# Kernel tuning notes

Hardware: AMD Instinct MI355X
Metric: run time of the kernel (lower is better)

Reference implementation:

```python
import jax, jax.numpy as jnp
import numpy as np

D_MODEL = 1024
EXPAND = 2
D_INNER = EXPAND * D_MODEL      # 2048
D_STATE = 2
D_CONV = 4
DT_RANK = (D_MODEL + 15) // 16  # 64
BATCH, SEQ = 2, 4096
LN_EPS = 1e-5


def setup_inputs() -> dict:
    key = jax.random.key(0)
    ks = jax.random.split(key, 16)
    s = 0.02
    inp = {
        "x":       jax.random.normal(ks[0], (BATCH, SEQ, D_MODEL), jnp.float32),
        # Mamba params (torch Linear convention: W is [out, in])
        "w_in":    jax.random.normal(ks[1], (2 * D_INNER, D_MODEL), jnp.float32) * s,
        "conv_w":  jax.random.normal(ks[2], (D_INNER, 1, D_CONV), jnp.float32) * s,
        "conv_b":  jnp.zeros((D_INNER,), jnp.float32),
        "w_xproj": jax.random.normal(ks[3], (DT_RANK + 2 * D_STATE, D_INNER), jnp.float32) * s,
        "w_dt":    jax.random.normal(ks[4], (D_INNER, DT_RANK), jnp.float32) * s,
        "b_dt":    jax.random.normal(ks[5], (D_INNER,), jnp.float32) * s - 4.0,  # softplus -> small dt
        "a_log":   jnp.log(jnp.broadcast_to(jnp.arange(1, D_STATE + 1, dtype=jnp.float32), (D_INNER, D_STATE))),
        "d_skip":  jnp.ones((D_INNER,), jnp.float32),
        "w_out":   jax.random.normal(ks[6], (D_MODEL, D_INNER), jnp.float32) * s,
        # LayerNorms
        "ln1_g":   jnp.ones((D_MODEL,), jnp.float32),
        "ln1_b":   jnp.zeros((D_MODEL,), jnp.float32),
        "ln2_g":   jnp.ones((D_MODEL,), jnp.float32),
        "ln2_b":   jnp.zeros((D_MODEL,), jnp.float32),
        # FFN (Linear d->d, ReLU, Linear d->d; dropout inactive at eval)
        "ffn_w1":  jax.random.normal(ks[7], (D_MODEL, D_MODEL), jnp.float32) * s,
        "ffn_b1":  jnp.zeros((D_MODEL,), jnp.float32),
        "ffn_w2":  jax.random.normal(ks[8], (D_MODEL, D_MODEL), jnp.float32) * s,
        "ffn_b2":  jnp.zeros((D_MODEL,), jnp.float32),
    }
    return inp


def _ln(x, g, b):
    mu = x.mean(-1, keepdims=True)
    v = ((x - mu) ** 2).mean(-1, keepdims=True)
    return (x - mu) * jax.lax.rsqrt(v + LN_EPS) * g + b


def _mamba(x, w_in, conv_w, conv_b, w_xproj, w_dt, b_dt, a_log, d_skip, w_out):
    Bsz = x.shape[0]
    xz = x @ w_in.T                      # (B,L,2*D_INNER)
    xp, z = jnp.split(xz, 2, axis=-1)
    # depthwise causal conv over time
    xc = jnp.transpose(xp, (0, 2, 1))    # (B,D,L)
    xc = jax.lax.conv_general_dilated(
        xc, conv_w, window_strides=(1,), padding=[(D_CONV - 1, 0)],
        feature_group_count=D_INNER)
    xc = xc + conv_b[None, :, None]
    xp = jax.nn.silu(jnp.transpose(xc, (0, 2, 1)))   # (B,L,D)
    # input-dependent SSM params
    x_dbl = xp @ w_xproj.T               # (B,L,DT_RANK+2N)
    dt, Bm, Cm = jnp.split(x_dbl, [DT_RANK, DT_RANK + D_STATE], axis=-1)
    dt = jax.nn.softplus(dt @ w_dt.T + b_dt)          # (B,L,D)
    A = -jnp.exp(a_log)                  # (D,N)
    dA = jnp.exp(dt[..., None] * A)                  # (B,L,D,N)
    dBu = dt[..., None] * Bm[:, :, None, :] * xp[..., None]  # (B,L,D,N)

    def step(h, inp):
        da, dbu, c = inp                 # (B,D,N),(B,D,N),(B,N)
        h = da * h + dbu
        y = jnp.einsum('bdn,bn->bd', h, c)
        return h, y

    h0 = jnp.zeros((Bsz, D_INNER, D_STATE), x.dtype)
    _, ys = jax.lax.scan(step, h0, (jnp.swapaxes(dA, 0, 1),
                                    jnp.swapaxes(dBu, 0, 1),
                                    jnp.swapaxes(Cm, 0, 1)))
    y = jnp.swapaxes(ys, 0, 1)           # (B,L,D)
    y = (y + d_skip * xp) * jax.nn.silu(z)
    return y @ w_out.T                   # (B,L,d_model)


def reference(x, w_in, conv_w, conv_b, w_xproj, w_dt, b_dt, a_log, d_skip, w_out,
              ln1_g, ln1_b, ln2_g, ln2_b, ffn_w1, ffn_b1, ffn_w2, ffn_b2):
    h = x + _mamba(_ln(x, ln1_g, ln1_b), w_in, conv_w, conv_b, w_xproj,
                   w_dt, b_dt, a_log, d_skip, w_out)
    f = _ln(h, ln2_g, ln2_b)
    f = jax.nn.relu(f @ ffn_w1.T + ffn_b1) @ ffn_w2.T + ffn_b2
    return h + f
```

## Files before the change

kernel.cpp:

```cpp
#include <hip/hip_runtime.h>

typedef unsigned short u16;
typedef __bf16 bf16x8 __attribute__((ext_vector_type(8)));
typedef float f32x4 __attribute__((ext_vector_type(4)));
typedef float f32x2 __attribute__((ext_vector_type(2)));
typedef u16 u16x4 __attribute__((ext_vector_type(4)));
typedef u16 u16x8 __attribute__((ext_vector_type(8)));

#define SEQ   4096
#define DM    1024
#define DI    2048
#define NTOK  8192
#define NXP   68
#define DTR   64
#define NCH   4096
#define CHUNK 32
#define NCHK  128

__device__ __forceinline__ float bf2f(u16 v) {
  union { unsigned u; float f; } x; x.u = ((unsigned)v) << 16; return x.f;
}
__device__ __forceinline__ u16 f2bf(float f) {
  unsigned u = __float_as_uint(f);
  return (u16)((u + 0x7FFFu + ((u >> 16) & 1u)) >> 16);
// ... 198 lines not shown
      bfr[j] = *reinterpret_cast<const bf16x8*>(
          &sB[cur][(wn + j * 16 + r) * 32 + (q ^ rsw) * 8]);
    if (kt + 1 < nk) {
      gA0 += 32; gA1 += 32; gB0 += 32; gB1 += 32;
      g2l16(gA0, lA0[cur ^ 1]); g2l16(gA1, lA1[cur ^ 1]);
      g2l16(gB0, lB0[cur ^ 1]); g2l16(gB1, lB1[cur ^ 1]);
    }
#pragma unroll
    for (int i = 0; i < 4; ++i)
#pragma unroll
      for (int j = 0; j < 4; ++j)
        acc[i][j] = __builtin_amdgcn_mfma_f32_16x16x32_bf16(af[i], bfr[j], acc[i][j], 0, 0, 0);
  }

  __syncthreads();
  float* ep = (wv < 2) ? ((float*)&sA[0][0] + wv * 2048)
                       : ((float*)&sB[0][0] + (wv - 2) * 2048);
  const int r2 = lane >> 2;
  const int ccol = ((lane & 3) ^ (r2 & 3)) * 16;

#pragma unroll
  for (int i = 0; i < 4; ++i) {
#pragma unroll
    for (int j = 0; j < 4; ++j)
#pragma unroll
      for (int t = 0; t < 4; ++t)
        ep[(q * 4 + t) * 68 + j * 16 + r] = acc[i][j][t];
    f32x4 w0 = *(const f32x4*)&ep[r2 * 68 + ccol + 0];
    f32x4 w1 = *(const f32x4*)&ep[r2 * 68 + ccol + 4];
    f32x4 w2 = *(const f32x4*)&ep[r2 * 68 + ccol + 8];
    f32x4 w3 = *(const f32x4*)&ep[r2 * 68 + ccol + 12];
    float vv[16];
#pragma unroll
    for (int k = 0; k < 4; ++k) {
      vv[k] = w0[k]; vv[4 + k] = w1[k]; vv[8 + k] = w2[k]; vv[12 + k] = w3[k];
    }
    const int row = m0 + wm + i * 16 + r2;
    const int colg = n0 + wn + ccol;
    const size_t idx = (size_t)row * N + colg;
    if (EPI == 2) {
      u16x8 b0 = *(const u16x8*)&bias[colg];
      u16x8 b1 = *(const u16x8*)&bias[colg + 8];
      u16x8 o0, o1;
#pragma unroll
      for (int k = 0; k < 8; ++k) {
        float v0 = vv[k] + bf2f(b0[k]);
        float v1 = vv[8 + k] + bf2f(b1[k]);
        v0 = (v0 > 15.f) ? v0 : __logf(1.f + __expf(v0));
        v1 = (v1 > 15.f) ? v1 : __logf(1.f + __expf(v1));
        o0[k] = f2bf(v0); o1[k] = f2bf(v1);
      }
      *(u16x8*)&((u16*)Cp)[idx] = o0;
      *(u16x8*)&((u16*)Cp)[idx + 8] = o1;
    } else if (EPI == 3) {
      float ax[16];
      if (fl) {
        f32x4 a0 = *(const f32x4*)&addf[idx];
        f32x4 a1 = *(const f32x4*)&addf[idx + 4];
        f32x4 a2 = *(const f32x4*)&addf[idx + 8];
        f32x4 a3 = *(const f32x4*)&addf[idx + 12];
#pragma unroll
        for (int k = 0; k < 4; ++k) {
          ax[k] = a0[k]; ax[4 + k] = a1[k]; ax[8 + k] = a2[k]; ax[12 + k] = a3[k];
        }
      } else {
        u16x8 a0 = *(const u16x8*)&addbf[idx];
        u16x8 a1 = *(const u16x8*)&addbf[idx + 8];
#pragma unroll
        for (int k = 0; k < 8; ++k) { ax[k] = bf2f(a0[k]); ax[8 + k] = bf2f(a1[k]); }
      }
      u16x8 o0, o1;
#pragma unroll
      for (int k = 0; k < 8; ++k) {
        o0[k] = f2bf(vv[k] + ax[k]); o1[k] = f2bf(vv[8 + k] + ax[8 + k]);
      }
      *(u16x8*)&((u16*)Cp)[idx] = o0;
      *(u16x8*)&((u16*)Cp)[idx + 8] = o1;
    } else if (EPI == 4) {
      u16x8 b0 = *(const u16x8*)&bias[colg];
      u16x8 b1 = *(const u16x8*)&bias[colg + 8];
      u16x8 o0, o1;
#pragma unroll
      for (int k = 0; k < 8; ++k) {
        o0[k] = f2bf(fmaxf(vv[k] + bf2f(b0[k]), 0.f));
        o1[k] = f2bf(fmaxf(vv[8 + k] + bf2f(b1[k]), 0.f));
      }
      *(u16x8*)&((u16*)Cp)[idx] = o0;
      *(u16x8*)&((u16*)Cp)[idx + 8] = o1;
    } else {
      u16x8 b0 = *(const u16x8*)&bias[colg];
      u16x8 b1 = *(const u16x8*)&bias[colg + 8];
      u16x8 a0 = *(const u16x8*)&addbf[idx];
      u16x8 a1 = *(const u16x8*)&addbf[idx + 8];
      float r0[8], r1[8];
#pragma unroll
      for (int k = 0; k < 8; ++k) {
        r0[k] = vv[k] + bf2f(b0[k]) + bf2f(a0[k]);
        r1[k] = vv[8 + k] + bf2f(b1[k]) + bf2f(a1[k]);
      }
      if (fl) {
        f32x4 f0, f1, f2, f3;
#pragma unroll
        for (int k = 0; k < 4; ++k) { f0[k] = r0[k]; f1[k] = r0[4 + k]; f2[k] = r1[k]; f3[k] = r1[4 + k]; }
        *(f32x4*)&((float*)Cp)[idx] = f0;
        *(f32x4*)&((float*)Cp)[idx + 4] = f1;
        *(f32x4*)&((float*)Cp)[idx + 8] = f2;
        *(f32x4*)&((float*)Cp)[idx + 12] = f3;
      } else {
        u16x8 o0, o1;
#pragma unroll
        for (int k = 0; k < 8; ++k) { o0[k] = f2bf(r0[k]); o1[k] = f2bf(r1[k]); }
        *(u16x8*)&((u16*)Cp)[idx] = o0;
        *(u16x8*)&((u16*)Cp)[idx + 8] = o1;
      }
    }
  }
}

template<int EPI, int LNBX>
__global__ __launch_bounds__(512, 2)
void gemm256_kernel(const u16* __restrict__ A, const u16* __restrict__ Bc,
                    const u16* __restrict__ Braw, int M, int N, int K,
                    const int* __restrict__ dtflag, void* __restrict__ Cp,
                    void* __restrict__ Cp2)
{
  __shared__ __align__(16) u16 sAB[2][2][2][128 * 64];
  (void)M;
  const int fl = *dtflag;
  const u16* __restrict__ B = fl ? Bc : Braw;
  const int tid = threadIdx.x;
  const int w = tid >> 6;
  const int lane = tid & 63;
  const int b = blockIdx.x;
  const int wg = (b & 7) * (gridDim.x >> 3) + (b >> 3);
  const int bx = wg & ((1 << LNBX) - 1);
  const int by = wg >> LNBX;
  const int m0 = by * 256;
  const int n0 = bx * 256;
  const int wm = w >> 2;
  const int wn = w & 3;
  const int r = lane & 15;
  const int q = lane >> 4;
  const int r7 = r & 7;
  const int srow = lane >> 3;
  const int schunk = ((lane & 7) ^ (srow & 7)) << 3;

  auto stageA = [&](int buf, int half, int kt) {
#pragma unroll
    for (int j = 0; j < 2; ++j) {
      u16* l = &sAB[buf][0][half][(w * 16 + j * 8) * 64];
      const u16* g = A + (size_t)(m0 + half * 128 + w * 16 + j * 8 + srow) * K
                       + (kt << 6) + schunk;
      g2l16(g, l);
    }
  };
  auto stageB = [&](int buf, int half, int kt) {
#pragma unroll
    for (int j = 0; j < 2; ++j) {
      u16* l = &sAB[buf][1][half][(w * 16 + j * 8) * 64];
      const u16* g = B + (size_t)(n0 + half * 128 + w * 16 + j * 8 + srow) * K
                       + (kt << 6) + schunk;
      g2l16(g, l);
    }
  };

  f32x4 acc[8][4];
#pragma unroll
  for (int i = 0; i < 8; ++i)
#pragma unroll
    for (int j = 0; j < 4; ++j)
#pragma unroll
      for (int t = 0; t < 4; ++t) acc[i][j][t] = 0.f;

  const int nk = K >> 6;
  stageA(0, 0, 0); stageA(0, 1, 0); stageB(0, 0, 0); stageB(0, 1, 0);
  if (nk > 1) { stageB(1, 0, 1); stageB(1, 1, 1); }
  if (nk > 1) asm volatile("s_waitcnt vmcnt(4)" ::: "memory");
  else        asm volatile("s_waitcnt vmcnt(0)" ::: "memory");
  SBAR0();
  __builtin_amdgcn_s_barrier();
  SBAR0();

  for (int kt = 0; kt < nk; ++kt) {
    const int c = kt & 1;
    const u16* bA = &sAB[c][0][wm][0];
    const u16* bB = &sAB[c][1][wn >> 1][0];
    const int rB = (wn & 1) * 64;
    bf16x8 af03[4][2], af47[4][2], b01[2][2], b23[2][2];

#pragma unroll
    for (int mf = 0; mf < 4; ++mf)
#pragma unroll
      for (int ks = 0; ks < 2; ++ks)
        af03[mf][ks] = *(const bf16x8*)&bA[(mf * 16 + r) * 64
                          + ((((ks << 2) + q) ^ r7) << 3)];
#pragma unroll
    for (int nf = 0; nf < 2; ++nf)
#pragma unroll
      for (int ks = 0; ks < 2; ++ks)
        b01[nf][ks] = *(const bf16x8*)&bB[(rB + nf * 16 + r) * 64
                          + ((((ks << 2) + q) ^ r7) << 3)];
    if (kt + 1 < nk) stageA(c ^ 1, 0, kt + 1);
    SBAR0(); __builtin_amdgcn_s_barrier();
    asm volatile("s_waitcnt lgkmcnt(0)" ::: "memory"); SBAR0();
    __builtin_amdgcn_s_setprio(1);
#pragma unroll
    for (int mf = 0; mf < 4; ++mf)
#pragma unroll
      for (int nf = 0; nf < 2; ++nf)
#pragma unroll
        for (int ks = 0; ks < 2; ++ks)
          acc[mf][nf] = __builtin_amdgcn_mfma_f32_16x16x32_bf16(
              af03[mf][ks], b01[nf][ks], acc[mf][nf], 0, 0, 0);
    __builtin_amdgcn_s_setprio(0);
    SBAR0(); __builtin_amdgcn_s_barrier(); SBAR0();

#pragma unroll
    for (int nf = 0; nf < 2; ++nf)
#pragma unroll
      for (int ks = 0; ks < 2; ++ks)
        b23[nf][ks] = *(const bf16x8*)&bB[(rB + (nf + 2) * 16 + r) * 64
                          + ((((ks << 2) + q) ^ r7) << 3)];
    if (kt + 1 < nk) stageA(c ^ 1, 1, kt + 1);
    SBAR0(); __builtin_amdgcn_s_barrier();
    asm volatile("s_waitcnt lgkmcnt(0)" ::: "memory"); SBAR0();
    __builtin_amdgcn_s_setprio(1);
#pragma unroll
    for (int mf = 0; mf < 4; ++mf)
#pragma unroll
      for (int nf = 0; nf < 2; ++nf)
#pragma unroll
        for (int ks = 0; ks < 2; ++ks)
          acc[mf][nf + 2] = __builtin_amdgcn_mfma_f32_16x16x32_bf16(
              af03[mf][ks], b23[nf][ks], acc[mf][nf + 2], 0, 0, 0);
    __builtin_amdgcn_s_setprio(0);
    SBAR0(); __builtin_amdgcn_s_barrier(); SBAR0();

#pragma unroll
    for (int mf = 0; mf < 4; ++mf)
#pragma unroll
      for (int ks = 0; ks < 2; ++ks)
        af47[mf][ks] = *(const bf16x8*)&bA[((mf + 4) * 16 + r) * 64
                          + ((((ks << 2) + q) ^ r7) << 3)];
    if (kt + 2 < nk) stageB(c, 0, kt + 2);
    SBAR0(); __builtin_amdgcn_s_barrier();
    asm volatile("s_waitcnt lgkmcnt(0)" ::: "memory"); SBAR0();
    __builtin_amdgcn_s_setprio(1);
#pragma unroll
    for (int mf = 0; mf < 4; ++mf)
#pragma unroll
      for (int nf = 0; nf < 2; ++nf)
#pragma unroll
        for (int ks = 0; ks < 2; ++ks)
          acc[mf + 4][nf + 2] = __builtin_amdgcn_mfma_f32_16x16x32_bf16(
              af47[mf][ks], b23[nf][ks], acc[mf + 4][nf + 2], 0, 0, 0);
    __builtin_amdgcn_s_setprio(0);
    SBAR0(); __builtin_amdgcn_s_barrier(); SBAR0();

    if (kt + 2 < nk) stageB(c, 1, kt + 2);
    SBAR0(); __builtin_amdgcn_s_barrier(); SBAR0();
    __builtin_amdgcn_s_setprio(1);
#pragma unroll
    for (int mf = 0; mf < 4; ++mf)
#pragma unroll
      for (int nf = 0; nf < 2; ++nf)
#pragma unroll
        for (int ks = 0; ks < 2; ++ks)
          acc[mf + 4][nf] = __builtin_amdgcn_mfma_f32_16x16x32_bf16(
              af47[mf][ks], b01[nf][ks], acc[mf + 4][nf], 0, 0, 0);
    __builtin_amdgcn_s_setprio(0);
    SBAR0();
    if (kt + 2 < nk) asm volatile("s_waitcnt vmcnt(4)" ::: "memory");
    else             asm volatile("s_waitcnt vmcnt(0)" ::: "memory");
    SBAR0();
    __builtin_amdgcn_s_barrier();
    SBAR0();
  }

  float* ep = (float*)&sAB[0][0][0][0] + w * 4096;
  const int r2 = lane >> 2;
  const int ccol = ((lane & 3) ^ (r2 & 3)) * 16;
  u16* C6 = (n0 < DI) ? (u16*)Cp : (u16*)Cp2;
  const int c6off = (n0 < DI) ? 0 : DI;
#pragma unroll
  for (int mf = 0; mf < 8; ++mf) {
#pragma unroll
    for (int nf = 0; nf < 4; ++nf)
#pragma unroll
      for (int t = 0; t < 4; ++t)
        ep[(q * 4 + t) * 68 + nf * 16 + r] = acc[mf][nf][t];
    f32x4 w0 = *(const f32x4*)&ep[r2 * 68 + ccol + 0];
    f32x4 w1 = *(const f32x4*)&ep[r2 * 68 + ccol + 4];
    f32x4 w2 = *(const f32x4*)&ep[r2 * 68 + ccol + 8];
    f32x4 w3 = *(const f32x4*)&ep[r2 * 68 + ccol + 12];
    u16x8 o0, o1;
#pragma unroll
    for (int k = 0; k < 4; ++k) {
      o0[k] = f2bf(w0[k]); o0[4 + k] = f2bf(w1[k]);
      o1[k] = f2bf(w2[k]); o1[4 + k] = f2bf(w3[k]);
    }
    const int row = m0 + wm * 128 + mf * 16 + r2;
    const int colg = n0 + wn * 64 + ccol;
    const size_t cb = (size_t)row * DI + (colg - c6off);
    *(u16x8*)&C6[cb] = o0;
    *(u16x8*)&C6[cb + 8] = o1;
  }
}

__global__ __launch_bounds__(256, 2)
void xproj_splitk(const u16* __restrict__ A, const u16* __restrict__ Bc,
                  const u16* __restrict__ Braw, const int* __restrict__ dtflag,
                  float* __restrict__ part)
{
  __shared__ __align__(16) u16 sA[2][128 * 32];
  __shared__ __align__(16) u16 sB[2][128 * 32];
  const int fl = *dtflag;
  const u16* __restrict__ B = fl ? Bc : Braw;
  const int tid = threadIdx.x;
  const int kz = blockIdx.x;
  const int m0 = blockIdx.y * 128;
  const int kbase = kz * 256;
  const int lane = tid & 63;
  const int wv = tid >> 6;
  const int wm = (wv & 1) * 64;
  const int wn = (wv >> 1) * 64;
  const int r = lane & 15;
  const int q = lane >> 4;
  const int rsw = (r >> 1) & 3;
  const int pr = lane >> 2;
  const int kc = (lane & 3) ^ ((pr >> 1) & 3);
  const int pk = kc * 8;

  u16* lA0[2] = { &sA[0][(wv * 2 + 0) * 512], &sA[1][(wv * 2 + 0) * 512] };
  u16* lA1[2] = { &sA[0][(wv * 2 + 1) * 512], &sA[1][(wv * 2 + 1) * 512] };
  u16* lB0[2] = { &sB[0][(wv * 2 + 0) * 512], &sB[1][(wv * 2 + 0) * 512] };
  u16* lB1[2] = { &sB[0][(wv * 2 + 1) * 512], &sB[1][(wv * 2 + 1) * 512] };
  int br0 = wv * 32 + pr;      if (br0 > 67) br0 = 67;
  int br1 = wv * 32 + 16 + pr; if (br1 > 67) br1 = 67;
  const u16* gA0 = A + (size_t)(m0 + wv * 32 + pr) * DI + kbase + pk;
  const u16* gA1 = gA0 + (size_t)16 * DI;
  const u16* gB0 = B + (size_t)br0 * DI + kbase + pk;
  const u16* gB1 = B + (size_t)br1 * DI + kbase + pk;

  f32x4 acc[4][4];
#pragma unroll
  for (int i = 0; i < 4; ++i)
#pragma unroll
    for (int j = 0; j < 4; ++j)
#pragma unroll
      for (int t = 0; t < 4; ++t) acc[i][j][t] = 0.f;

  g2l16(gA0, lA0[0]); g2l16(gA1, lA1[0]);
  g2l16(gB0, lB0[0]); g2l16(gB1, lB1[0]);

  for (int kt = 0; kt < 8; ++kt) {
    const int cur = kt & 1;
    __syncthreads();
    bf16x8 af[4], bfr[4];
// ... 29 lines not shown
          part[((size_t)kz * NTOK + row) * NXP + col] = acc[i][j][t];
      }
}

__global__ __launch_bounds__(256)
void xreduce_kernel(const float* __restrict__ part, u16* __restrict__ dtraw,
                    float* __restrict__ bc)
{
  const int i = blockIdx.x * 256 + threadIdx.x;
  if (i >= NTOK * NXP) return;
  const int row = i / NXP, col = i - row * NXP;
  float s = 0.f;
#pragma unroll
  for (int z = 0; z < 8; ++z) s += part[(size_t)z * NTOK * NXP + i];
  if (col < DTR) dtraw[(size_t)row * DTR + col] = f2bf(s);
  else           bc[row * 4 + (col - DTR)] = s;
}

__global__ __launch_bounds__(256)
void conv_silu_kernel(const u16* __restrict__ xp, const u16* __restrict__ cwT,
                      const u16* __restrict__ cb, u16* __restrict__ u)
{
  const int token = blockIdx.x;
  const int t = token & (SEQ - 1);
  const int d0 = threadIdx.x * 8;
  const ptrdiff_t base = (ptrdiff_t)token * DI + d0;
  float acc[8];
  u16x8 cbv = *(const u16x8*)(cb + d0);
#pragma unroll
  for (int k = 0; k < 8; ++k) acc[k] = bf2f(cbv[k]);
#pragma unroll
  for (int j = 0; j < 4; ++j) {
    if (t - 3 + j >= 0) {
      u16x8 xv = *(const u16x8*)(xp + base + (ptrdiff_t)(j - 3) * DI);
      u16x8 wv = *(const u16x8*)(cwT + j * DI + d0);
#pragma unroll
      for (int k = 0; k < 8; ++k) acc[k] += bf2f(wv[k]) * bf2f(xv[k]);
    }
  }
  u16x8 o;
#pragma unroll
  for (int k = 0; k < 8; ++k) {
    const float sg = 1.f / (1.f + __expf(-acc[k]));
    o[k] = f2bf(acc[k] * sg);
  }
  *(u16x8*)(u + base) = o;
}

__global__ __launch_bounds__(256)
void scan_pass1(const u16* __restrict__ dtb, const u16* __restrict__ ub,
                const float* __restrict__ bc, const u16* __restrict__ a_log,
                float* __restrict__ S, float* __restrict__ hf0, float* __restrict__ hf1)
{
  const int g4 = blockIdx.x * 256 + threadIdx.x;
  const int chg = g4 & (NCH / 4 - 1);
  const int c = g4 >> 10;
  const int ch0 = chg * 4;
  const int b = ch0 >> 11;
  const int d0 = ch0 & (DI - 1);
  u16x8 av = *(const u16x8*)(a_log + d0 * 2);
  float A0[4], A1[4];
#pragma unroll
  for (int k = 0; k < 4; ++k) {
    A0[k] = -__expf(bf2f(av[2 * k]));
    A1[k] = -__expf(bf2f(av[2 * k + 1]));
  }
  float h0[4] = {0.f, 0.f, 0.f, 0.f}, h1[4] = {0.f, 0.f, 0.f, 0.f};
  float s[4] = {0.f, 0.f, 0.f, 0.f};
  const int row0 = b * SEQ + c * CHUNK;
  for (int i = 0; i < CHUNK; ++i) {
    const size_t row = row0 + i;
    u16x4 dtv = *(const u16x4*)(dtb + row * DI + d0);
    u16x4 uv  = *(const u16x4*)(ub + row * DI + d0);
    f32x2 Bv = *(const f32x2*)(bc + row * 4);
#pragma unroll
    for (int k = 0; k < 4; ++k) {
      const float dt = bf2f(dtv[k]);
      const float dtu = dt * bf2f(uv[k]);
      h0[k] = __expf(A0[k] * dt) * h0[k] + dtu * Bv[0];
      h1[k] = __expf(A1[k] * dt) * h1[k] + dtu * Bv[1];
      s[k] += dt;
    }
  }
  const size_t g0 = (size_t)c * NCH + ch0;
  *(f32x4*)(S + g0)   = f32x4{s[0], s[1], s[2], s[3]};
  *(f32x4*)(hf0 + g0) = f32x4{h0[0], h0[1], h0[2], h0[3]};
  *(f32x4*)(hf1 + g0) = f32x4{h1[0], h1[1], h1[2], h1[3]};
}

__global__ __launch_bounds__(256)
void scan_pass2(const float* __restrict__ S, const float* __restrict__ hf0,
                const float* __restrict__ hf1, const u16* __restrict__ a_log,
                float* __restrict__ hi0, float* __restrict__ hi1)
{
  const int ch = blockIdx.x * 256 + threadIdx.x;
  const int d = ch & (DI - 1);
  const float A0 = -__expf(bf2f(a_log[d * 2 + 0]));
  const float A1 = -__expf(bf2f(a_log[d * 2 + 1]));
  float h0 = 0.f, h1 = 0.f;
  size_t g = ch;
  float sv = S[g], f0 = hf0[g], f1 = hf1[g];
  for (int c = 0; c < NCHK; ++c) {
    float svn = 0.f, f0n = 0.f, f1n = 0.f;
    if (c + 1 < NCHK) {
      const size_t gn = g + NCH;
      svn = S[gn]; f0n = hf0[gn]; f1n = hf1[gn];
    }
    hi0[g] = h0; hi1[g] = h1;
    h0 = __expf(A0 * sv) * h0 + f0;
    h1 = __expf(A1 * sv) * h1 + f1;
    sv = svn; f0 = f0n; f1 = f1n;
    g += NCH;
  }
}

__global__ __launch_bounds__(256)
void scan_pass3(const u16* __restrict__ dtb, const u16* __restrict__ ub,
                const float* __restrict__ bc, const u16* __restrict__ zbuf,
                const u16* __restrict__ a_log, const u16* __restrict__ d_skip,
                const float* __restrict__ hi0, const float* __restrict__ hi1,
                u16* __restrict__ yb)
{
  const int g4 = blockIdx.x * 256 + threadIdx.x;
  const int chg = g4 & (NCH / 4 - 1);
  const int c = g4 >> 10;
  const int ch0 = chg * 4;
  const int b = ch0 >> 11;
  const int d0 = ch0 & (DI - 1);
  u16x8 av = *(const u16x8*)(a_log + d0 * 2);
  u16x4 dkv = *(const u16x4*)(d_skip + d0);
  float A0[4], A1[4], dsk[4];
#pragma unroll
  for (int k = 0; k < 4; ++k) {
    A0[k] = -__expf(bf2f(av[2 * k]));
    A1[k] = -__expf(bf2f(av[2 * k + 1]));
    dsk[k] = bf2f(dkv[k]);
  }
  const size_t g0 = (size_t)c * NCH + ch0;
  f32x4 h0v = *(const f32x4*)(hi0 + g0);
  f32x4 h1v = *(const f32x4*)(hi1 + g0);
  float h0[4], h1[4];
#pragma unroll
  for (int k = 0; k < 4; ++k) { h0[k] = h0v[k]; h1[k] = h1v[k]; }
  const int row0 = b * SEQ + c * CHUNK;
  for (int i = 0; i < CHUNK; ++i) {
    const size_t row = row0 + i;
    u16x4 dtv = *(const u16x4*)(dtb + row * DI + d0);
    u16x4 uv  = *(const u16x4*)(ub + row * DI + d0);
    u16x4 zv  = *(const u16x4*)(zbuf + row * DI + d0);
    f32x4 bcv = *(const f32x4*)(bc + row * 4);
    u16x4 o;
#pragma unroll
    for (int k = 0; k < 4; ++k) {
      const float dt = bf2f(dtv[k]);
      const float uu = bf2f(uv[k]);
      const float dtu = dt * uu;
      h0[k] = __expf(A0[k] * dt) * h0[k] + dtu * bcv[0];
      h1[k] = __expf(A1[k] * dt) * h1[k] + dtu * bcv[1];
      const float y = h0[k] * bcv[2] + h1[k] * bcv[3];
      const float z = bf2f(zv[k]);
      const float sz = z / (1.f + __expf(-z));
      o[k] = f2bf((y + dsk[k] * uu) * sz);
    }
    *(u16x4*)(yb + row * DI + d0) = o;
  }
}

extern "C" void kernel_launch(void* const* d_in, const int* in_sizes, int n_in,
                              void* d_out, int out_size, void* d_ws, size_t ws_size,
                              hipStream_t stream)
{
  const void* x       = d_in[0];
  const void* w_in    = d_in[1];
  const void* conv_w  = d_in[2];
  const void* conv_b  = d_in[3];
  const void* w_xproj = d_in[4];
  const void* w_dt    = d_in[5];
  const void* b_dt    = d_in[6];
  const void* a_log   = d_in[7];
  const void* d_skip  = d_in[8];
  const void* w_out   = d_in[9];
  const void* ln1_g   = d_in[10];
  const void* ln1_b   = d_in[11];
  const void* ln2_g   = d_in[12];
  const void* ln2_b   = d_in[13];
  const void* ffn_w1  = d_in[14];
  const void* ffn_b1  = d_in[15];
  const void* ffn_w2  = d_in[16];
  const void* ffn_b2  = d_in[17];
  char* ws = (char*)d_ws;

  const size_t o_flag  = 0;
  const size_t o_small = 256;
  const size_t o_cwout = o_small + 65536;
  const size_t o_cff1  = o_cwout + (size_t)DM * DI * 2;
  const size_t o_cff2  = o_cff1  + (size_t)DM * DM * 2;
  const size_t o_cxp   = o_cff2  + (size_t)DM * DM * 2;
  const size_t o_cwdt  = o_cxp   + (size_t)NXP * DI * 2;
  const size_t o_xn    = 9437184;
  const size_t o_xp    = o_xn + (size_t)NTOK * DM * 2;
  const size_t o_z     = o_xp + (size_t)NTOK * DI * 2;
  const size_t o_u     = o_z  + (size_t)NTOK * DI * 2;
  const size_t o_bc    = o_u  + (size_t)NTOK * DI * 2;
  const size_t SCN = (size_t)NCHK * NCH * 4;
  const size_t o_S   = o_xn + 0 * SCN;
  const size_t o_hf0 = o_xn + 1 * SCN;
  const size_t o_hf1 = o_xn + 2 * SCN;
  const size_t o_hi0 = o_xn + 3 * SCN;
  const size_t o_hi1 = o_xn + 4 * SCN;

  int*   flagp   = (int*)(ws + o_flag);
  u16*   csmall  = (u16*)(ws + o_small);
  u16*   c_cwT   = csmall +     0;
  u16*   c_convb = csmall +  8192;
  u16*   c_bdt   = csmall + 10240;
  u16*   c_alog  = csmall + 12288;
  u16*   c_dskip = csmall + 16384;
  u16*   c_ln1g  = csmall + 18432;
  u16*   c_ln1b  = csmall + 19456;
  u16*   c_ln2g  = csmall + 20480;
  u16*   c_ln2b  = csmall + 21504;
  u16*   c_fb1   = csmall + 22528;
  u16*   c_fb2   = csmall + 23552;
  u16*   c_wout  = (u16*)(ws + o_cwout);
  u16*   c_ff1   = (u16*)(ws + o_cff1);
  u16*   c_ff2   = (u16*)(ws + o_cff2);
  u16*   c_xproj = (u16*)(ws + o_cxp);
  u16*   c_wdt   = (u16*)(ws + o_cwdt);
  u16*   c_win   = (u16*)(ws + o_u);
  u16*   xn      = (u16*)(ws + o_xn);
  u16*   xp      = (u16*)(ws + o_xp);
  u16*   zb      = (u16*)(ws + o_z);
  u16*   u       = (u16*)(ws + o_u);
  float* part    = (float*)(ws + o_xp);
  u16*   dtraw   = (u16*)(ws + o_xn);
  u16*   dtb     = xp;
  u16*   yb      = xp;
  float* bc      = (float*)(ws + o_bc);
  float* S       = (float*)(ws + o_S);
  float* hf0     = (float*)(ws + o_hf0);
  float* hf1     = (float*)(ws + o_hf1);
  float* hi0     = (float*)(ws + o_hi0);
  float* hi1     = (float*)(ws + o_hi1);
  u16*   hb      = (u16*)(ws + o_z);
  u16*   hn      = (u16*)(ws + o_xn);
  u16*   f1      = (u16*)(ws + o_u);

  const dim3 blk(256);

  detect_kernel<<<1, blk, 0, stream>>>((const u16*)x, flagp);
  convert_all<<<NBB + 96, blk, 0, stream>>>(
      (const float*)w_in, (const float*)w_xproj, (const float*)w_dt,
      (const float*)w_out, (const float*)ffn_w1, (const float*)ffn_w2,
      c_win, c_xproj, c_wdt, c_wout, c_ff1, c_ff2,
      conv_w, conv_b, b_dt, a_log, d_skip,
      ln1_g, ln1_b, ln2_g, ln2_b, ffn_b1, ffn_b2,
      csmall, flagp);

  ln_kernel<0><<<NTOK / 2, blk, 0, stream>>>(x, c_ln1g, c_ln1b, xn, flagp);
  gemm256_kernel<6, 4><<<512, dim3(512), 0, stream>>>(
      xn, c_win, (const u16*)w_in, NTOK, 2 * DI, DM, flagp, xp, zb);
  conv_silu_kernel<<<NTOK, blk, 0, stream>>>(xp, c_cwT, c_convb, u);
  xproj_splitk<<<dim3(8, 64), blk, 0, stream>>>(u, c_xproj, (const u16*)w_xproj,
                                                flagp, part);
  xreduce_kernel<<<(NTOK * NXP + 255) / 256, blk, 0, stream>>>(part, dtraw, bc);
  gemm_kernel<2, 4><<<1024, blk, 0, stream>>>(dtraw, c_wdt, (const u16*)w_dt,
                                              NTOK, DI, DTR,
                                              c_bdt, nullptr, nullptr, flagp, dtb, nullptr);
  scan_pass1<<<NCHK * NCH / 4 / 256, blk, 0, stream>>>(dtb, u, bc, c_alog, S, hf0, hf1);
  scan_pass2<<<NCH / 256, blk, 0, stream>>>(S, hf0, hf1, c_alog, hi0, hi1);
  scan_pass3<<<NCHK * NCH / 4 / 256, blk, 0, stream>>>(dtb, u, bc, zb, c_alog, c_dskip,
                                                       hi0, hi1, yb);
  gemm_kernel<3, 3><<<512, blk, 0, stream>>>(yb, c_wout, (const u16*)w_out,
                                             NTOK, DM, DI,
                                             nullptr, (const u16*)x, (const float*)x,
                                             flagp, hb, nullptr);
  ln_kernel<1><<<NTOK / 2, blk, 0, stream>>>(hb, c_ln2g, c_ln2b, hn, flagp);
  gemm_kernel<4, 3><<<512, blk, 0, stream>>>(hn, c_ff1, (const u16*)ffn_w1,
                                             NTOK, DM, DM,
                                             c_fb1, nullptr, nullptr, flagp, f1, nullptr);
  gemm_kernel<5, 3><<<512, blk, 0, stream>>>(f1, c_ff2, (const u16*)ffn_w2,
                                             NTOK, DM, DM,
                                             c_fb2, hb, nullptr, flagp, d_out, nullptr);
}
```

Baseline: 463.4 us.

## Replace 256-tile GEMM with 128-tile double-buffered GEMM and widen scan per-thread channels

Replaces the 512-thread 256x256 in-projection GEMM with a 256-thread 128x128 double-buffered kernel. That kernel is also used for the out-projection and both FFN GEMMs, with their epilogues moved into it. Scan passes 1 and 3 now handle 8 channels per thread and prefetch the next row's inputs into registers to hide load latency. The smaller tile increases global traffic per FLOP for the large in-projection but gives more blocks and a simpler schedule. Wider scan threads halve the grid and raise register pressure.

```diff
diff --git a/kernel.cpp b/kernel.cpp
--- a/kernel.cpp
+++ b/kernel.cpp
@@ -274,157 +274,92 @@
       }
       *(u16x8*)&((u16*)Cp)[idx] = o0;
       *(u16x8*)&((u16*)Cp)[idx + 8] = o1;
-    } else if (EPI == 3) {
-      float ax[16];
-      if (fl) {
-        f32x4 a0 = *(const f32x4*)&addf[idx];
-        f32x4 a1 = *(const f32x4*)&addf[idx + 4];
-        f32x4 a2 = *(const f32x4*)&addf[idx + 8];
-        f32x4 a3 = *(const f32x4*)&addf[idx + 12];
-#pragma unroll
-        for (int k = 0; k < 4; ++k) {
-          ax[k] = a0[k]; ax[4 + k] = a1[k]; ax[8 + k] = a2[k]; ax[12 + k] = a3[k];
-        }
-      } else {
-        u16x8 a0 = *(const u16x8*)&addbf[idx];
-        u16x8 a1 = *(const u16x8*)&addbf[idx + 8];
-#pragma unroll
-        for (int k = 0; k < 8; ++k) { ax[k] = bf2f(a0[k]); ax[8 + k] = bf2f(a1[k]); }
-      }
-      u16x8 o0, o1;
-#pragma unroll
-      for (int k = 0; k < 8; ++k) {
-        o0[k] = f2bf(vv[k] + ax[k]); o1[k] = f2bf(vv[8 + k] + ax[8 + k]);
-      }
-      *(u16x8*)&((u16*)Cp)[idx] = o0;
-      *(u16x8*)&((u16*)Cp)[idx + 8] = o1;
-    } else if (EPI == 4) {
-      u16x8 b0 = *(const u16x8*)&bias[colg];
-      u16x8 b1 = *(const u16x8*)&bias[colg + 8];
-      u16x8 o0, o1;
-#pragma unroll
-      for (int k = 0; k < 8; ++k) {
-        o0[k] = f2bf(fmaxf(vv[k] + bf2f(b0[k]), 0.f));
-        o1[k] = f2bf(fmaxf(vv[8 + k] + bf2f(b1[k]), 0.f));
-      }
-      *(u16x8*)&((u16*)Cp)[idx] = o0;
-      *(u16x8*)&((u16*)Cp)[idx + 8] = o1;
-    } else {
-      u16x8 b0 = *(const u16x8*)&bias[colg];
-      u16x8 b1 = *(const u16x8*)&bias[colg + 8];
-      u16x8 a0 = *(const u16x8*)&addbf[idx];
-      u16x8 a1 = *(const u16x8*)&addbf[idx + 8];
-      float r0[8], r1[8];
-#pragma unroll
-      for (int k = 0; k < 8; ++k) {
-        r0[k] = vv[k] + bf2f(b0[k]) + bf2f(a0[k]);
-        r1[k] = vv[8 + k] + bf2f(b1[k]) + bf2f(a1[k]);
-      }
-      if (fl) {
-        f32x4 f0, f1, f2, f3;
-#pragma unroll
-        for (int k = 0; k < 4; ++k) { f0[k] = r0[k]; f1[k] = r0[4 + k]; f2[k] = r1[k]; f3[k] = r1[4 + k]; }
-        *(f32x4*)&((float*)Cp)[idx] = f0;
-        *(f32x4*)&((float*)Cp)[idx + 4] = f1;
-        *(f32x4*)&((float*)Cp)[idx + 8] = f2;
-        *(f32x4*)&((float*)Cp)[idx + 12] = f3;
-      } else {
-        u16x8 o0, o1;
-#pragma unroll
-        for (int k = 0; k < 8; ++k) { o0[k] = f2bf(r0[k]); o1[k] = f2bf(r1[k]); }
-        *(u16x8*)&((u16*)Cp)[idx] = o0;
-        *(u16x8*)&((u16*)Cp)[idx + 8] = o1;
-      }
     }
   }
 }
 
 template<int EPI, int LNBX>
-__global__ __launch_bounds__(512, 2)
-void gemm256_kernel(const u16* __restrict__ A, const u16* __restrict__ Bc,
-                    const u16* __restrict__ Braw, int M, int N, int K,
-                    const int* __restrict__ dtflag, void* __restrict__ Cp,
-                    void* __restrict__ Cp2)
-{
-  __shared__ __align__(16) u16 sAB[2][2][2][128 * 64];
+__global__ __launch_bounds__(256, 2)
+void gemm_dp(const u16* __restrict__ A, const u16* __restrict__ Bc,
+             const u16* __restrict__ Braw, int M, int N, int K,
+             const u16* __restrict__ bias, const u16* __restrict__ addbf,
+             const float* __restrict__ addf, const int* __restrict__ dtflag,
+             void* __restrict__ Cp, void* __restrict__ Cp2)
+{
+  __shared__ __align__(16) u16 sA[2][128 * 64];
+  __shared__ __align__(16) u16 sB[2][128 * 64];
   (void)M;
   const int fl = *dtflag;
   const u16* __restrict__ B = fl ? Bc : Braw;
   const int tid = threadIdx.x;
+  const int lane = tid & 63;
   const int w = tid >> 6;
-  const int lane = tid & 63;
   const int b = blockIdx.x;
-  const int wg = (b & 7) * (gridDim.x >> 3) + (b >> 3);
+  const int wg = (b & 7) * ((int)gridDim.x >> 3) + (b >> 3);
   const int bx = wg & ((1 << LNBX) - 1);
   const int by = wg >> LNBX;
-  const int m0 = by * 256;
-  const int n0 = bx * 256;
-  const int wm = w >> 2;
-  const int wn = w & 3;
+  const int m0 = by * 128;
+  const int n0 = bx * 128;
+  const int wm = (w & 1) * 64;
+  const int wn = (w >> 1) * 64;
   const int r = lane & 15;
   const int q = lane >> 4;
-  const int r7 = r & 7;
+  const int r7 = lane & 7;
   const int srow = lane >> 3;
   const int schunk = ((lane & 7) ^ (srow & 7)) << 3;
 
-  auto stageA = [&](int buf, int half, int kt) {
-#pragma unroll
-    for (int j = 0; j < 2; ++j) {
-      u16* l = &sAB[buf][0][half][(w * 16 + j * 8) * 64];
-      const u16* g = A + (size_t)(m0 + half * 128 + w * 16 + j * 8 + srow) * K
-                       + (kt << 6) + schunk;
+  auto stage = [&](u16* dst, const u16* gbase, int ld) {
+#pragma unroll
+    for (int j = 0; j < 4; ++j) {
+      u16* l = dst + ((j * 4 + w) * 8) * 64;
+      const u16* g = gbase + (size_t)((j * 4 + w) * 8 + srow) * ld + schunk;
       g2l16(g, l);
     }
   };
-  auto stageB = [&](int buf, int half, int kt) {
-#pragma unroll
-    for (int j = 0; j < 2; ++j) {
-      u16* l = &sAB[buf][1][half][(w * 16 + j * 8) * 64];
-      const u16* g = B + (size_t)(n0 + half * 128 + w * 16 + j * 8 + srow) * K
-                       + (kt << 6) + schunk;
-      g2l16(g, l);
-    }
-  };
-
-  f32x4 acc[8][4];
-#pragma unroll
-  for (int i = 0; i < 8; ++i)
+  const u16* gA = A + (size_t)m0 * K;
+  const u16* gB = B + (size_t)n0 * K;
+
+  f32x4 acc[4][4];
+#pragma unroll
+  for (int i = 0; i < 4; ++i)
 #pragma unroll
     for (int j = 0; j < 4; ++j)
 #pragma unroll
       for (int t = 0; t < 4; ++t) acc[i][j][t] = 0.f;
 
   const int nk = K >> 6;
-  stageA(0, 0, 0); stageA(0, 1, 0); stageB(0, 0, 0); stageB(0, 1, 0);
-  if (nk > 1) { stageB(1, 0, 1); stageB(1, 1, 1); }
-  if (nk > 1) asm volatile("s_waitcnt vmcnt(4)" ::: "memory");
-  else        asm volatile("s_waitcnt vmcnt(0)" ::: "memory");
+  stage(&sA[0][0], gA, K);
+  stage(&sB[0][0], gB, K);
+  if (nk > 1) {
+    stage(&sA[1][0], gA + 64, K);
+    asm volatile("s_waitcnt vmcnt(4)" ::: "memory");
+  } else {
+    asm volatile("s_waitcnt vmcnt(0)" ::: "memory");
+  }
   SBAR0();
   __builtin_amdgcn_s_barrier();
   SBAR0();
 
   for (int kt = 0; kt < nk; ++kt) {
     const int c = kt & 1;
-    const u16* bA = &sAB[c][0][wm][0];
-    const u16* bB = &sAB[c][1][wn >> 1][0];
-    const int rB = (wn & 1) * 64;
-    bf16x8 af03[4][2], af47[4][2], b01[2][2], b23[2][2];
+    bf16x8 af[4][2], b01[2][2], b23[2][2];
 
 #pragma unroll
     for (int mf = 0; mf < 4; ++mf)
 #pragma unroll
       for (int ks = 0; ks < 2; ++ks)
-        af03[mf][ks] = *(const bf16x8*)&bA[(mf * 16 + r) * 64
-                          + ((((ks << 2) + q) ^ r7) << 3)];
+        af[mf][ks] = *(const bf16x8*)&sA[c][(wm + mf * 16 + r) * 64
+                        + ((((ks << 2) + q) ^ r7) << 3)];
 #pragma unroll
     for (int nf = 0; nf < 2; ++nf)
 #pragma unroll
       for (int ks = 0; ks < 2; ++ks)
-        b01[nf][ks] = *(const bf16x8*)&bB[(rB + nf * 16 + r) * 64
-                          + ((((ks << 2) + q) ^ r7) << 3)];
-    if (kt + 1 < nk) stageA(c ^ 1, 0, kt + 1);
-    SBAR0(); __builtin_amdgcn_s_barrier();
-    asm volatile("s_waitcnt lgkmcnt(0)" ::: "memory"); SBAR0();
+        b01[nf][ks] = *(const bf16x8*)&sB[c][(wn + nf * 16 + r) * 64
+                        + ((((ks << 2) + q) ^ r7) << 3)];
+    if (kt + 1 < nk) stage(&sB[c ^ 1][0], gB + (size_t)(kt + 1) * 64, K);
+    SBAR0();
+    __builtin_amdgcn_s_barrier();
+    SBAR0();
     __builtin_amdgcn_s_setprio(1);
 #pragma unroll
     for (int mf = 0; mf < 4; ++mf)
@@ -433,99 +368,132 @@
 #pragma unroll
         for (int ks = 0; ks < 2; ++ks)
           acc[mf][nf] = __builtin_amdgcn_mfma_f32_16x16x32_bf16(
-              af03[mf][ks], b01[nf][ks], acc[mf][nf], 0, 0, 0);
-    __builtin_amdgcn_s_setprio(0);
-    SBAR0(); __builtin_amdgcn_s_barrier(); SBAR0();
-
-#pragma unroll
-    for (int nf = 0; nf < 2; ++nf)
-#pragma unroll
-      for (int ks = 0; ks < 2; ++ks)
-        b23[nf][ks] = *(const bf16x8*)&bB[(rB + (nf + 2) * 16 + r) * 64
-                          + ((((ks << 2) + q) ^ r7) << 3)];
-    if (kt + 1 < nk) stageA(c ^ 1, 1, kt + 1);
-    SBAR0(); __builtin_amdgcn_s_barrier();
-    asm volatile("s_waitcnt lgkmcnt(0)" ::: "memory"); SBAR0();
-    __builtin_amdgcn_s_setprio(1);
-#pragma unroll
-    for (int mf = 0; mf < 4; ++mf)
-#pragma unroll
-      for (int nf = 0; nf < 2; ++nf)
-#pragma unroll
-        for (int ks = 0; ks < 2; ++ks)
-          acc[mf][nf + 2] = __builtin_amdgcn_mfma_f32_16x16x32_bf16(
-              af03[mf][ks], b23[nf][ks], acc[mf][nf + 2], 0, 0, 0);
-    __builtin_amdgcn_s_setprio(0);
-    SBAR0(); __builtin_amdgcn_s_barrier(); SBAR0();
-
-#pragma unroll
-    for (int mf = 0; mf < 4; ++mf)
-#pragma unroll
-      for (int ks = 0; ks < 2; ++ks)
-        af47[mf][ks] = *(const bf16x8*)&bA[((mf + 4) * 16 + r) * 64
-                          + ((((ks << 2) + q) ^ r7) << 3)];
-    if (kt + 2 < nk) stageB(c, 0, kt + 2);
-    SBAR0(); __builtin_amdgcn_s_barrier();
-    asm volatile("s_waitcnt lgkmcnt(0)" ::: "memory"); SBAR0();
-    __builtin_amdgcn_s_setprio(1);
-#pragma unroll
-    for (int mf = 0; mf < 4; ++mf)
-#pragma unroll
-      for (int nf = 0; nf < 2; ++nf)
-#pragma unroll
-        for (int ks = 0; ks < 2; ++ks)
-          acc[mf + 4][nf + 2] = __builtin_amdgcn_mfma_f32_16x16x32_bf16(
-              af47[mf][ks], b23[nf][ks], acc[mf + 4][nf + 2], 0, 0, 0);
-    __builtin_amdgcn_s_setprio(0);
-    SBAR0(); __builtin_amdgcn_s_barrier(); SBAR0();
-
-    if (kt + 2 < nk) stageB(c, 1, kt + 2);
-    SBAR0(); __builtin_amdgcn_s_barrier(); SBAR0();
-    __builtin_amdgcn_s_setprio(1);
-#pragma unroll
-    for (int mf = 0; mf < 4; ++mf)
-#pragma unroll
-      for (int nf = 0; nf < 2; ++nf)
-#pragma unroll
-        for (int ks = 0; ks < 2; ++ks)
-          acc[mf + 4][nf] = __builtin_amdgcn_mfma_f32_16x16x32_bf16(
-              af47[mf][ks], b01[nf][ks], acc[mf + 4][nf], 0, 0, 0);
+              af[mf][ks], b01[nf][ks], acc[mf][nf], 0, 0, 0);
     __builtin_amdgcn_s_setprio(0);
     SBAR0();
+
+#pragma unroll
+    for (int nf = 0; nf < 2; ++nf)
+#pragma unroll
+      for (int ks = 0; ks < 2; ++ks)
+        b23[nf][ks] = *(const bf16x8*)&sB[c][(wn + (nf + 2) * 16 + r) * 64
+                        + ((((ks << 2) + q) ^ r7) << 3)];
+    if (kt + 2 < nk) stage(&sA[c][0], gA + (size_t)(kt + 2) * 64, K);
     if (kt + 2 < nk) asm volatile("s_waitcnt vmcnt(4)" ::: "memory");
     else             asm volatile("s_waitcnt vmcnt(0)" ::: "memory");
     SBAR0();
     __builtin_amdgcn_s_barrier();
     SBAR0();
-  }
-
-  float* ep = (float*)&sAB[0][0][0][0] + w * 4096;
+    __builtin_amdgcn_s_setprio(1);
+#pragma unroll
+    for (int mf = 0; mf < 4; ++mf)
+#pragma unroll
+      for (int nf = 0; nf < 2; ++nf)
+#pragma unroll
+        for (int ks = 0; ks < 2; ++ks)
+          acc[mf][nf + 2] = __builtin_amdgcn_mfma_f32_16x16x32_bf16(
+              af[mf][ks], b23[nf][ks], acc[mf][nf + 2], 0, 0, 0);
+    __builtin_amdgcn_s_setprio(0);
+    SBAR0();
+  }
+
+  __syncthreads();
+  float* ep = (w < 2) ? ((float*)&sA[0][0] + w * 2048)
+                      : ((float*)&sB[0][0] + (w - 2) * 2048);
   const int r2 = lane >> 2;
   const int ccol = ((lane & 3) ^ (r2 & 3)) * 16;
-  u16* C6 = (n0 < DI) ? (u16*)Cp : (u16*)Cp2;
-  const int c6off = (n0 < DI) ? 0 : DI;
-#pragma unroll
-  for (int mf = 0; mf < 8; ++mf) {
-#pragma unroll
-    for (int nf = 0; nf < 4; ++nf)
+  u16* C6 = nullptr; int c6off = 0;
+  if (EPI == 6) { C6 = (n0 < DI) ? (u16*)Cp : (u16*)Cp2; c6off = (n0 < DI) ? 0 : DI; }
+#pragma unroll
+  for (int i = 0; i < 4; ++i) {
+#pragma unroll
+    for (int j = 0; j < 4; ++j)
 #pragma unroll
       for (int t = 0; t < 4; ++t)
-        ep[(q * 4 + t) * 68 + nf * 16 + r] = acc[mf][nf][t];
+        ep[(q * 4 + t) * 68 + j * 16 + r] = acc[i][j][t];
     f32x4 w0 = *(const f32x4*)&ep[r2 * 68 + ccol + 0];
     f32x4 w1 = *(const f32x4*)&ep[r2 * 68 + ccol + 4];
     f32x4 w2 = *(const f32x4*)&ep[r2 * 68 + ccol + 8];
     f32x4 w3 = *(const f32x4*)&ep[r2 * 68 + ccol + 12];
-    u16x8 o0, o1;
+    float vv[16];
 #pragma unroll
     for (int k = 0; k < 4; ++k) {
-      o0[k] = f2bf(w0[k]); o0[4 + k] = f2bf(w1[k]);
-      o1[k] = f2bf(w2[k]); o1[4 + k] = f2bf(w3[k]);
-    }
-    const int row = m0 + wm * 128 + mf * 16 + r2;
-    const int colg = n0 + wn * 64 + ccol;
-    const size_t cb = (size_t)row * DI + (colg - c6off);
-    *(u16x8*)&C6[cb] = o0;
-    *(u16x8*)&C6[cb + 8] = o1;
+      vv[k] = w0[k]; vv[4 + k] = w1[k]; vv[8 + k] = w2[k]; vv[12 + k] = w3[k];
+    }
+    const int row = m0 + wm + i * 16 + r2;
+    const int colg = n0 + wn + ccol;
+    if (EPI == 6) {
+      u16x8 o0, o1;
+#pragma unroll
+      for (int k = 0; k < 8; ++k) { o0[k] = f2bf(vv[k]); o1[k] = f2bf(vv[8 + k]); }
+      const size_t cb = (size_t)row * DI + (colg - c6off);
+      *(u16x8*)&C6[cb] = o0;
+      *(u16x8*)&C6[cb + 8] = o1;
+    } else {
+      const size_t idx = (size_t)row * N + colg;
+      if (EPI == 3) {
+        float ax[16];
+        if (fl) {
+          f32x4 a0 = *(const f32x4*)&addf[idx];
+          f32x4 a1 = *(const f32x4*)&addf[idx + 4];
+          f32x4 a2 = *(const f32x4*)&addf[idx + 8];
+          f32x4 a3 = *(const f32x4*)&addf[idx + 12];
+#pragma unroll
+          for (int k = 0; k < 4; ++k) {
+            ax[k] = a0[k]; ax[4 + k] = a1[k]; ax[8 + k] = a2[k]; ax[12 + k] = a3[k];
+          }
+        } else {
+          u16x8 a0 = *(const u16x8*)&addbf[idx];
+          u16x8 a1 = *(const u16x8*)&addbf[idx + 8];
+#pragma unroll
+          for (int k = 0; k < 8; ++k) { ax[k] = bf2f(a0[k]); ax[8 + k] = bf2f(a1[k]); }
+        }
+        u16x8 o0, o1;
+#pragma unroll
+        for (int k = 0; k < 8; ++k) {
+          o0[k] = f2bf(vv[k] + ax[k]); o1[k] = f2bf(vv[8 + k] + ax[8 + k]);
+        }
+        *(u16x8*)&((u16*)Cp)[idx] = o0;
+        *(u16x8*)&((u16*)Cp)[idx + 8] = o1;
+      } else if (EPI == 4) {
+        u16x8 b0 = *(const u16x8*)&bias[colg];
+        u16x8 b1 = *(const u16x8*)&bias[colg + 8];
+        u16x8 o0, o1;
+#pragma unroll
+        for (int k = 0; k < 8; ++k) {
+          o0[k] = f2bf(fmaxf(vv[k] + bf2f(b0[k]), 0.f));
+          o1[k] = f2bf(fmaxf(vv[8 + k] + bf2f(b1[k]), 0.f));
+        }
+        *(u16x8*)&((u16*)Cp)[idx] = o0;
+        *(u16x8*)&((u16*)Cp)[idx + 8] = o1;
+      } else {
+        u16x8 b0 = *(const u16x8*)&bias[colg];
+        u16x8 b1 = *(const u16x8*)&bias[colg + 8];
+        u16x8 a0 = *(const u16x8*)&addbf[idx];
+        u16x8 a1 = *(const u16x8*)&addbf[idx + 8];
+        float r0[8], r1[8];
+#pragma unroll
+        for (int k = 0; k < 8; ++k) {
+          r0[k] = vv[k] + bf2f(b0[k]) + bf2f(a0[k]);
+          r1[k] = vv[8 + k] + bf2f(b1[k]) + bf2f(a1[k]);
+        }
+        if (fl) {
+          f32x4 f0, f1, f2, f3;
+#pragma unroll
+          for (int k = 0; k < 4; ++k) { f0[k] = r0[k]; f1[k] = r0[4 + k]; f2[k] = r1[k]; f3[k] = r1[4 + k]; }
+          *(f32x4*)&((float*)Cp)[idx] = f0;
+          *(f32x4*)&((float*)Cp)[idx + 4] = f1;
+          *(f32x4*)&((float*)Cp)[idx + 8] = f2;
+          *(f32x4*)&((float*)Cp)[idx + 12] = f3;
+        } else {
+          u16x8 o0, o1;
+#pragma unroll
+          for (int k = 0; k < 8; ++k) { o0[k] = f2bf(r0[k]); o1[k] = f2bf(r1[k]); }
+          *(u16x8*)&((u16*)Cp)[idx] = o0;
+          *(u16x8*)&((u16*)Cp)[idx + 8] = o1;
+        }
+      }
+    }
   }
 }
 
@@ -661,40 +629,54 @@
                 const float* __restrict__ bc, const u16* __restrict__ a_log,
                 float* __restrict__ S, float* __restrict__ hf0, float* __restrict__ hf1)
 {
-  const int g4 = blockIdx.x * 256 + threadIdx.x;
-  const int chg = g4 & (NCH / 4 - 1);
-  const int c = g4 >> 10;
-  const int ch0 = chg * 4;
+  const int g8 = blockIdx.x * 256 + threadIdx.x;
+  const int chg = g8 & (NCH / 8 - 1);
+  const int c = g8 >> 9;
+  const int ch0 = chg * 8;
   const int b = ch0 >> 11;
   const int d0 = ch0 & (DI - 1);
-  u16x8 av = *(const u16x8*)(a_log + d0 * 2);
-  float A0[4], A1[4];
+  u16x8 av0 = *(const u16x8*)(a_log + d0 * 2);
+  u16x8 av1 = *(const u16x8*)(a_log + d0 * 2 + 8);
+  float A0[8], A1[8];
 #pragma unroll
   for (int k = 0; k < 4; ++k) {
-    A0[k] = -__expf(bf2f(av[2 * k]));
-    A1[k] = -__expf(bf2f(av[2 * k + 1]));
-  }
-  float h0[4] = {0.f, 0.f, 0.f, 0.f}, h1[4] = {0.f, 0.f, 0.f, 0.f};
-  float s[4] = {0.f, 0.f, 0.f, 0.f};
+    A0[k]     = -__expf(bf2f(av0[2 * k]));
+    A1[k]     = -__expf(bf2f(av0[2 * k + 1]));
+    A0[4 + k] = -__expf(bf2f(av1[2 * k]));
+    A1[4 + k] = -__expf(bf2f(av1[2 * k + 1]));
+  }
+  float h0[8], h1[8], s[8];
+#pragma unroll
+  for (int k = 0; k < 8; ++k) { h0[k] = 0.f; h1[k] = 0.f; s[k] = 0.f; }
   const int row0 = b * SEQ + c * CHUNK;
+  u16x8 dtv = *(const u16x8*)(dtb + (size_t)row0 * DI + d0);
+  u16x8 uv  = *(const u16x8*)(ub  + (size_t)row0 * DI + d0);
+  f32x2 Bv  = *(const f32x2*)(bc + (size_t)row0 * 4);
   for (int i = 0; i < CHUNK; ++i) {
-    const size_t row = row0 + i;
-    u16x4 dtv = *(const u16x4*)(dtb + row * DI + d0);
-    u16x4 uv  = *(const u16x4*)(ub + row * DI + d0);
-    f32x2 Bv = *(const f32x2*)(bc + row * 4);
-#pragma unroll
-    for (int k = 0; k < 4; ++k) {
+    u16x8 dtn, un; f32x2 Bn;
+    if (i + 1 < CHUNK) {
+      const size_t rn = row0 + i + 1;
+      dtn = *(const u16x8*)(dtb + rn * DI + d0);
+      un  = *(const u16x8*)(ub + rn * DI + d0);
+      Bn  = *(const f32x2*)(bc + rn * 4);
+    }
+#pragma unroll
+    for (int k = 0; k < 8; ++k) {
       const float dt = bf2f(dtv[k]);
       const float dtu = dt * bf2f(uv[k]);
       h0[k] = __expf(A0[k] * dt) * h0[k] + dtu * Bv[0];
       h1[k] = __expf(A1[k] * dt) * h1[k] + dtu * Bv[1];
       s[k] += dt;
     }
+    dtv = dtn; uv = un; Bv = Bn;
   }
   const size_t g0 = (size_t)c * NCH + ch0;
-  *(f32x4*)(S + g0)   = f32x4{s[0], s[1], s[2], s[3]};
-  *(f32x4*)(hf0 + g0) = f32x4{h0[0], h0[1], h0[2], h0[3]};
-  *(f32x4*)(hf1 + g0) = f32x4{h1[0], h1[1], h1[2], h1[3]};
+  *(f32x4*)(S + g0)       = f32x4{s[0], s[1], s[2], s[3]};
+  *(f32x4*)(S + g0 + 4)   = f32x4{s[4], s[5], s[6], s[7]};
+  *(f32x4*)(hf0 + g0)     = f32x4{h0[0], h0[1], h0[2], h0[3]};
+  *(f32x4*)(hf0 + g0 + 4) = f32x4{h0[4], h0[5], h0[6], h0[7]};
+  *(f32x4*)(hf1 + g0)     = f32x4{h1[0], h1[1], h1[2], h1[3]};
+  *(f32x4*)(hf1 + g0 + 4) = f32x4{h1[4], h1[5], h1[6], h1[7]};
 }
 
 __global__ __launch_bounds__(256)
@@ -730,37 +712,53 @@
                 const float* __restrict__ hi0, const float* __restrict__ hi1,
                 u16* __restrict__ yb)
 {
-  const int g4 = blockIdx.x * 256 + threadIdx.x;
-  const int chg = g4 & (NCH / 4 - 1);
-  const int c = g4 >> 10;
-  const int ch0 = chg * 4;
+  const int g8 = blockIdx.x * 256 + threadIdx.x;
+  const int chg = g8 & (NCH / 8 - 1);
+  const int c = g8 >> 9;
+  const int ch0 = chg * 8;
   const int b = ch0 >> 11;
   const int d0 = ch0 & (DI - 1);
-  u16x8 av = *(const u16x8*)(a_log + d0 * 2);
-  u16x4 dkv = *(const u16x4*)(d_skip + d0);
-  float A0[4], A1[4], dsk[4];
+  u16x8 av0 = *(const u16x8*)(a_log + d0 * 2);
+  u16x8 av1 = *(const u16x8*)(a_log + d0 * 2 + 8);
+  u16x8 dkv = *(const u16x8*)(d_skip + d0);
+  float A0[8], A1[8], dsk[8];
 #pragma unroll
   for (int k = 0; k < 4; ++k) {
-    A0[k] = -__expf(bf2f(av[2 * k]));
-    A1[k] = -__expf(bf2f(av[2 * k + 1]));
-    dsk[k] = bf2f(dkv[k]);
-  }
+    A0[k]     = -__expf(bf2f(av0[2 * k]));
+    A1[k]     = -__expf(bf2f(av0[2 * k + 1]));
+    A0[4 + k] = -__expf(bf2f(av1[2 * k]));
+    A1[4 + k] = -__expf(bf2f(av1[2 * k + 1]));
+  }
+#pragma unroll
+  for (int k = 0; k < 8; ++k) dsk[k] = bf2f(dkv[k]);
   const size_t g0 = (size_t)c * NCH + ch0;
-  f32x4 h0v = *(const f32x4*)(hi0 + g0);
-  f32x4 h1v = *(const f32x4*)(hi1 + g0);
-  float h0[4], h1[4];
-#pragma unroll
-  for (int k = 0; k < 4; ++k) { h0[k] = h0v[k]; h1[k] = h1v[k]; }
+  f32x4 h0a = *(const f32x4*)(hi0 + g0);
+  f32x4 h0b = *(const f32x4*)(hi0 + g0 + 4);
+  f32x4 h1a = *(const f32x4*)(hi1 + g0);
+  f32x4 h1b = *(const f32x4*)(hi1 + g0 + 4);
+  float h0[8], h1[8];
+#pragma unroll
+  for (int k = 0; k < 4; ++k) {
+    h0[k] = h0a[k]; h0[4 + k] = h0b[k];
+    h1[k] = h1a[k]; h1[4 + k] = h1b[k];
+  }
   const int row0 = b * SEQ + c * CHUNK;
+  u16x8 dtv = *(const u16x8*)(dtb + (size_t)row0 * DI + d0);
+  u16x8 uv  = *(const u16x8*)(ub  + (size_t)row0 * DI + d0);
+  u16x8 zv  = *(const u16x8*)(zbuf + (size_t)row0 * DI + d0);
+  f32x4 bcv = *(const f32x4*)(bc + (size_t)row0 * 4);
   for (int i = 0; i < CHUNK; ++i) {
-    const size_t row = row0 + i;
-    u16x4 dtv = *(const u16x4*)(dtb + row * DI + d0);
-    u16x4 uv  = *(const u16x4*)(ub + row * DI + d0);
-    u16x4 zv  = *(const u16x4*)(zbuf + row * DI + d0);
-    f32x4 bcv = *(const f32x4*)(bc + row * 4);
-    u16x4 o;
-#pragma unroll
-    for (int k = 0; k < 4; ++k) {
+    u16x8 dtn, un, zn; f32x4 bn;
+    if (i + 1 < CHUNK) {
+      const size_t rn = row0 + i + 1;
+      dtn = *(const u16x8*)(dtb + rn * DI + d0);
+      un  = *(const u16x8*)(ub + rn * DI + d0);
+      zn  = *(const u16x8*)(zbuf + rn * DI + d0);
+      bn  = *(const f32x4*)(bc + rn * 4);
+    }
+    u16x8 o;
+#pragma unroll
+    for (int k = 0; k < 8; ++k) {
       const float dt = bf2f(dtv[k]);
       const float uu = bf2f(uv[k]);
       const float dtu = dt * uu;
@@ -771,7 +769,8 @@
       const float sz = z / (1.f + __expf(-z));
       o[k] = f2bf((y + dsk[k] * uu) * sz);
     }
-    *(u16x4*)(yb + row * DI + d0) = o;
+    *(u16x8*)(yb + (size_t)(row0 + i) * DI + d0) = o;
+    dtv = dtn; uv = un; zv = zn; bcv = bn;
   }
 }
 
@@ -867,8 +866,9 @@
       csmall, flagp);
 
   ln_kernel<0><<<NTOK / 2, blk, 0, stream>>>(x, c_ln1g, c_ln1b, xn, flagp);
-  gemm256_kernel<6, 4><<<512, dim3(512), 0, stream>>>(
-      xn, c_win, (const u16*)w_in, NTOK, 2 * DI, DM, flagp, xp, zb);
+  gemm_dp<6, 5><<<2048, blk, 0, stream>>>(xn, c_win, (const u16*)w_in,
+                                          NTOK, 2 * DI, DM,
+                                          nullptr, nullptr, nullptr, flagp, xp, zb);
   conv_silu_kernel<<<NTOK, blk, 0, stream>>>(xp, c_cwT, c_convb, u);
   xproj_splitk<<<dim3(8, 64), blk, 0, stream>>>(u, c_xproj, (const u16*)w_xproj,
                                                 flagp, part);
@@ -876,19 +876,19 @@
   gemm_kernel<2, 4><<<1024, blk, 0, stream>>>(dtraw, c_wdt, (const u16*)w_dt,
                                               NTOK, DI, DTR,
                                               c_bdt, nullptr, nullptr, flagp, dtb, nullptr);
-  scan_pass1<<<NCHK * NCH / 4 / 256, blk, 0, stream>>>(dtb, u, bc, c_alog, S, hf0, hf1);
+  scan_pass1<<<NCHK * NCH / 8 / 256, blk, 0, stream>>>(dtb, u, bc, c_alog, S, hf0, hf1);
   scan_pass2<<<NCH / 256, blk, 0, stream>>>(S, hf0, hf1, c_alog, hi0, hi1);
-  scan_pass3<<<NCHK * NCH / 4 / 256, blk, 0, stream>>>(dtb, u, bc, zb, c_alog, c_dskip,
+  scan_pass3<<<NCHK * NCH / 8 / 256, blk, 0, stream>>>(dtb, u, bc, zb, c_alog, c_dskip,
                                                        hi0, hi1, yb);
-  gemm_kernel<3, 3><<<512, blk, 0, stream>>>(yb, c_wout, (const u16*)w_out,
-                                             NTOK, DM, DI,
-                                             nullptr, (const u16*)x, (const float*)x,
-                                             flagp, hb, nullptr);
+  gemm_dp<3, 3><<<512, blk, 0, stream>>>(yb, c_wout, (const u16*)w_out,
+                                         NTOK, DM, DI,
+                                         nullptr, (const u16*)x, (const float*)x,
+                                         flagp, hb, nullptr);
   ln_kernel<1><<<NTOK / 2, blk, 0, stream>>>(hb, c_ln2g, c_ln2b, hn, flagp);
-  gemm_kernel<4, 3><<<512, blk, 0, stream>>>(hn, c_ff1, (const u16*)ffn_w1,
-                                             NTOK, DM, DM,
-                                             c_fb1, nullptr, nullptr, flagp, f1, nullptr);
-  gemm_kernel<5, 3><<<512, blk, 0, stream>>>(f1, c_ff2, (const u16*)ffn_w2,
-                                             NTOK, DM, DM,
-                                             c_fb2, hb, nullptr, flagp, d_out, nullptr);
-}
+  gemm_dp<4, 3><<<512, blk, 0, stream>>>(hn, c_ff1, (const u16*)ffn_w1,
+                                         NTOK, DM, DM,
+                                         c_fb1, nullptr, nullptr, flagp, f1, nullptr);
+  gemm_dp<5, 3><<<512, blk, 0, stream>>>(f1, c_ff2, (const u16*)ffn_w2,
+                                         NTOK, DM, DM,
+                                         c_fb2, hb, nullptr, flagp, d_out, nullptr);
+}
```

After: 459.1 us. No clear change (-0.9%).
